# Kernel optimization log

Hardware: AMD Instinct MI355X
Metric: run time of the kernel (lower is better)

The kernel has to match this reference:

```python
import jax, jax.numpy as jnp
import numpy as np

B, T, V, E, M, L = 1024, 64, 1024, 512, 1024, 32
PE, PO = M // 2, (M - 1) // 2  # even/odd pair counts


def complex_normalize(x, eps=1e-8):
    mag = jnp.sqrt((x.real ** 2 + x.imag ** 2).sum(-1, keepdims=True) + eps)
    return x / mag


def pair_unitary(v0, v1, t, p, r):
    # 2x2 MZI unitary applied to pairs (v0, v1); t/p/r are (P,) broadcast over batch
    c, s = jnp.cos(t), jnp.sin(t)
    eip, eir = jnp.exp(1j * p), jnp.exp(1j * r)
    u11 = eip * c * eir
    u12 = eip * (1j * s)
    u21 = (1j * s) * eir
    u22 = c
    return u11 * v0 + u12 * v1, u21 * v0 + u22 * v1


def setup_inputs() -> dict:
    key = jax.random.key(0)
    ks = jax.random.split(key, 16)
    sE = 1.0 / np.sqrt(E)
    return {
        "context_tokens": jax.random.randint(ks[0], (B, T), 0, V),
        "embed": 0.02 * jax.random.normal(ks[1], (V, E), jnp.float32),
        "W_ih": sE * jax.random.normal(ks[2], (3 * E, E), jnp.float32),
        "W_hh": sE * jax.random.normal(ks[3], (3 * E, E), jnp.float32),
        "b_ih": jnp.zeros((3 * E,), jnp.float32),
        "b_hh": jnp.zeros((3 * E,), jnp.float32),
        "Wc": 0.02 * jax.random.normal(ks[4], (2 * M, E), jnp.float32),
        "bc": jnp.zeros((2 * M,), jnp.float32),
        "phase": 0.1 * jax.random.normal(ks[5], (L, M), jnp.float32),
        "theta_e": 0.1 * jax.random.normal(ks[6], (L, PE), jnp.float32),
        "phi_e": 0.1 * jax.random.normal(ks[7], (L, PE), jnp.float32),
        "rho_e": 0.1 * jax.random.normal(ks[8], (L, PE), jnp.float32),
        "theta_o": 0.1 * jax.random.normal(ks[9], (L, PO), jnp.float32),
        "phi_o": 0.1 * jax.random.normal(ks[10], (L, PO), jnp.float32),
        "rho_o": 0.1 * jax.random.normal(ks[11], (L, PO), jnp.float32),
        "R_real": 0.01 * jax.random.normal(ks[12], (V, M), jnp.float32),
        "R_imag": 0.01 * jax.random.normal(ks[13], (V, M), jnp.float32),
    }


def reference(context_tokens, embed, W_ih, W_hh, b_ih, b_hh, Wc, bc,
              phase, theta_e, phi_e, rho_e, theta_o, phi_o, rho_o,
              R_real, R_imag):
    # --- ContextEncoder: embedding + GRU (torch gate order r,z,n) ---
    x = embed[context_tokens]                      # (B,T,E)
    x_gates = x @ W_ih.T + b_ih                    # (B,T,3E) precomputed input gates

    def gru_step(h, xg):
        ir, iz, in_ = jnp.split(xg, 3, axis=-1)
        hr, hz, hn = jnp.split(h @ W_hh.T + b_hh, 3, axis=-1)
        r = jax.nn.sigmoid(ir + hr)
        z = jax.nn.sigmoid(iz + hz)
        n = jnp.tanh(in_ + r * hn)
        return (1.0 - z) * n + z * h, None

    h0 = jnp.zeros((x.shape[0], embed.shape[1]), x.dtype)
    h, _ = jax.lax.scan(gru_step, h0, jnp.swapaxes(x_gates, 0, 1))  # (B,E)

    zc = h @ Wc.T + bc                              # (B,2M)
    re, im = jnp.split(zc, 2, axis=-1)
    psi = complex_normalize(re + 1j * im)           # (B,M) complex64

    # --- QuantumCore: stack of MZI layers ---
    def layer(psi, p):
        ph, te, pe, re_, to, po, ro = p
        psi = psi * jnp.exp(1j * ph)
        D = psi.shape[1]
        # even pairs (0,1),(2,3),...
        v0, v1 = pair_unitary(psi[:, 0::2], psi[:, 1::2], te, pe, re_)
        psi = psi.at[:, 0::2].set(v0).at[:, 1::2].set(v1)
        # odd pairs (1,2),(3,4),...
        v0, v1 = pair_unitary(psi[:, 1:D - 1:2], psi[:, 2:D:2], to, po, ro)
        psi = psi.at[:, 1:D - 1:2].set(v0).at[:, 2:D:2].set(v1)
        return complex_normalize(psi), None

    psi, _ = jax.lax.scan(layer, psi, (phase, theta_e, phi_e, rho_e,
                                       theta_o, phi_o, rho_o))

    # --- QuantumReadout: Born rule log-probs ---
    R = R_real + 1j * R_imag                        # (V,M)
    amps = psi @ R.T                                # (B,V) complex
    log_mag_sq = jnp.log(amps.real ** 2 + amps.imag ** 2 + 1e-12)
    return log_mag_sq - jax.scipy.special.logsumexp(log_mag_sq, axis=-1, keepdims=True)
```

## Files before the change

### kernel.cpp

```cpp
#include <hip/hip_runtime.h>
#include <math.h>

typedef __bf16 bf16_t;
typedef bf16_t bf16x8 __attribute__((ext_vector_type(8)));
typedef float  f32x4  __attribute__((ext_vector_type(4)));

#define B_  1024
#define T_  64
#define V_  1024
#define E_  512
#define M_  1024
#define L_  32
#define PE_ 512
#define PO_ 511
#define G3_ 1536
#define M2_ 2048

#define MFMA_BF16 __builtin_amdgcn_mfma_f32_16x16x32_bf16

__device__ __forceinline__ void stage16f(float* lds_base, const float* gsrc) {
  __builtin_amdgcn_global_load_lds(
      (const __attribute__((address_space(1))) unsigned int*)gsrc,
      (__attribute__((address_space(3))) unsigned int*)lds_base, 16, 0, 0);
}

__device__ __forceinline__ size_t tiled_off(int row, int k) {
  return ((size_t)(row >> 4) * 16 + (k >> 5)) * 512 +
         (size_t)(((k >> 3) & 3) * 16 + (row & 15)) * 8 + (k & 7);
}

__device__ __forceinline__ void split_chunk(const float* __restrict__ src,
                                            bf16_t* __restrict__ hi,
                                            bf16_t* __restrict__ lo, int blk,
                                            int tid) {
  int i4 = (blk * 256 + tid) * 4;
  float4 v = *(const float4*)&src[i4];
  float vv[4] = {v.x, v.y, v.z, v.w};
#pragma unroll
  for (int j = 0; j < 4; j++) {
    bf16_t h = (bf16_t)vv[j];
    hi[i4 + j] = h;
    lo[i4 + j] = (bf16_t)(vv[j] - (float)h);
  }
}

__global__ __launch_bounds__(256) void prep_all(
    const float* __restrict__ embed, bf16_t* __restrict__ emb_hi,
    bf16_t* __restrict__ emb_lo, const float* __restrict__ W_ih,
    bf16_t* __restrict__ wih_hi, bf16_t* __restrict__ wih_lo,
    const float* __restrict__ Wc, bf16_t* __restrict__ wc_hi,
    bf16_t* __restrict__ wc_lo, const float* __restrict__ R_real,
    bf16_t* __restrict__ rr_hi, bf16_t* __restrict__ rr_lo,
    const float* __restrict__ R_imag, bf16_t* __restrict__ ri_hi,
    bf16_t* __restrict__ ri_lo, const float* __restrict__ W_hh,
    bf16_t* __restrict__ Wp_hi, bf16_t* __restrict__ Wp_lo,
    const float* __restrict__ phase, const float* __restrict__ th_e,
    const float* __restrict__ ph_e, const float* __restrict__ rh_e,
    float* __restrict__ Uep, const float* __restrict__ th_o,
    const float* __restrict__ ph_o, const float* __restrict__ rh_o,
    float* __restrict__ Uop) {
  const int bid = blockIdx.x, tid = threadIdx.x;
  if (bid < 512) {
    split_chunk(embed, emb_hi, emb_lo, bid, tid);
  } else if (bid < 1280) {
    split_chunk(W_ih, wih_hi, wih_lo, bid - 512, tid);
  } else if (bid < 2304) {
    split_chunk(Wc, wc_hi, wc_lo, bid - 1280, tid);
  } else if (bid < 3328) {
    split_chunk(R_real, rr_hi, rr_lo, bid - 2304, tid);
  } else if (bid < 4352) {
    split_chunk(R_imag, ri_hi, ri_lo, bid - 3328, tid);
  } else if (bid < 5888) {
    int q = bid - 4352;
    int c = q / 96, loc = q % 96;
    int g = loc >> 5, el = loc & 31;
    const float* src = &W_hh[(size_t)(g * 512 + c * 32 + el) * 512];
    if (tid < 64) {
      int k0 = tid * 8;
      float4 v0 = *(const float4*)&src[k0];
      float4 v1 = *(const float4*)&src[k0 + 4];
      float vv[8] = {v0.x, v0.y, v0.z, v0.w, v1.x, v1.y, v1.z, v1.w};
      bf16x8 h8, l8;
#pragma unroll
      for (int j = 0; j < 8; j++) {
        bf16_t h = (bf16_t)vv[j];
        h8[j] = h;
        l8[j] = (bf16_t)(vv[j] - (float)h);
      }
      size_t toff = tiled_off(q, k0);
      *(bf16x8*)&Wp_hi[toff] = h8;
      *(bf16x8*)&Wp_lo[toff] = l8;
    }
  } else if (bid < 5952) {
    int idx = (bid - 5888) * 256 + tid;
    if (idx < L_ * PE_) {
      int l = idx >> 9, p = idx & 511;
      float t = th_e[idx], pp = ph_e[idx], r = rh_e[idx];
      float c = cosf(t), s = sinf(t);
      float cp = cosf(pp), sp = sinf(pp), cr = cosf(r), sr = sinf(r);
      float u11r = c * (cp * cr - sp * sr), u11i = c * (cp * sr + sp * cr);
      float u12r = -s * sp, u12i = s * cp;
      float u21r = -s * sr, u21i = s * cr;
      float u22r = c, u22i = 0.0f;
      float f0 = phase[l * M_ + 2 * p], f1 = phase[l * M_ + 2 * p + 1];
      float c0 = cosf(f0), s0 = sinf(f0), c1 = cosf(f1), s1 = sinf(f1);
      float a, b;
      a = u11r * c0 - u11i * s0; b = u11r * s0 + u11i * c0; u11r = a; u11i = b;
      a = u21r * c0 - u21i * s0; b = u21r * s0 + u21i * c0; u21r = a; u21i = b;
      a = u12r * c1 - u12i * s1; b = u12r * s1 + u12i * c1; u12r = a; u12i = b;
      a = u22r * c1 - u22i * s1; b = u22r * s1 + u22i * c1; u22r = a; u22i = b;
      int j = p & 3, ln = (p >> 2) & 63, hh = p >> 8;
      size_t base = (size_t)l * 4096 + (size_t)(j * 4 + hh) * 256 + ln * 4;
      *(float4*)&Uep[base]       = make_float4(u11r, u11i, u12r, u12i);
      *(float4*)&Uep[base + 512] = make_float4(u21r, u21i, u22r, u22i);
    }
  } else {
    int idx = (bid - 5952) * 256 + tid;
    if (idx < L_ * PO_) {
      int l = idx / PO_, p = idx % PO_;
      float t = th_o[idx], pp = ph_o[idx], r = rh_o[idx];
      float c = cosf(t), s = sinf(t);
      float cp = cosf(pp), sp = sinf(pp), cr = cosf(r), sr = sinf(r);
      int j = p & 3, ln = (p >> 2) & 63, hh = p >> 8;
      size_t base = (size_t)l * 4096 + (size_t)(j * 4 + hh) * 256 + ln * 4;
      *(float4*)&Uop[base] = make_float4(c * (cp * cr - sp * sr),
                                         c * (cp * sr + sp * cr), -s * sp,
                                         s * cp);
      *(float4*)&Uop[base + 512] = make_float4(-s * sr, s * cr, c, 0.0f);
    }
  }
}

__global__ __launch_bounds__(256) void gemm_bt_mfma_split(
    const bf16_t* __restrict__ Ah, const bf16_t* __restrict__ Al,
    const bf16_t* __restrict__ Bh, const bf16_t* __restrict__ Bl,
    float* __restrict__ C, int Ndim, int K) {
  __shared__ bf16_t sAh[64 * 32], sAl[64 * 32], sBh[64 * 32], sBl[64 * 32];
  const int tid = threadIdx.x;
  const int m0 = blockIdx.y * 64, n0 = blockIdx.x * 64;
  const int wave = tid >> 6, lane = tid & 63;
  const int wr = wave >> 1, wc = wave & 1;
  const int quad = lane >> 4, l16 = lane & 15;
  f32x4 acc[2][2] = {};
  const int srow = tid >> 2, sk = (tid & 3) * 8;

  for (int k0 = 0; k0 < K; k0 += 32) {
    bf16x8 ah = *(const bf16x8*)&Ah[(size_t)(m0 + srow) * K + k0 + sk];
    bf16x8 al = *(const bf16x8*)&Al[(size_t)(m0 + srow) * K + k0 + sk];
    bf16x8 bh = *(const bf16x8*)&Bh[(size_t)(n0 + srow) * K + k0 + sk];
    bf16x8 bl = *(const bf16x8*)&Bl[(size_t)(n0 + srow) * K + k0 + sk];
    __syncthreads();
    *(bf16x8*)&sAh[srow * 32 + sk] = ah;
    *(bf16x8*)&sAl[srow * 32 + sk] = al;
    *(bf16x8*)&sBh[srow * 32 + sk] = bh;
    *(bf16x8*)&sBl[srow * 32 + sk] = bl;
    __syncthreads();
    bf16x8 fAh[2], fAl[2], fBh[2], fBl[2];
#pragma unroll
    for (int i = 0; i < 2; i++) {
      fAh[i] = *(const bf16x8*)&sAh[(wr * 32 + i * 16 + l16) * 32 + quad * 8];
      fAl[i] = *(const bf16x8*)&sAl[(wr * 32 + i * 16 + l16) * 32 + quad * 8];
      fBh[i] = *(const bf16x8*)&sBh[(wc * 32 + i * 16 + l16) * 32 + quad * 8];
      fBl[i] = *(const bf16x8*)&sBl[(wc * 32 + i * 16 + l16) * 32 + quad * 8];
    }
#pragma unroll
    for (int i = 0; i < 2; i++)
#pragma unroll
      for (int j = 0; j < 2; j++) {
        acc[i][j] = MFMA_BF16(fAh[i], fBh[j], acc[i][j], 0, 0, 0);
        acc[i][j] = MFMA_BF16(fAh[i], fBl[j], acc[i][j], 0, 0, 0);
        acc[i][j] = MFMA_BF16(fAl[i], fBh[j], acc[i][j], 0, 0, 0);
      }
  }
#pragma unroll
  for (int i = 0; i < 2; i++)
#pragma unroll
    for (int j = 0; j < 2; j++)
#pragma unroll
      for (int r = 0; r < 4; r++) {
        int row = wr * 32 + i * 16 + quad * 4 + r;
        int col = wc * 32 + j * 16 + l16;
        C[(size_t)(m0 + row) * Ndim + n0 + col] = acc[i][j][r];
      }
}

__global__ __launch_bounds__(512) void gru_step10(
    const bf16_t* __restrict__ Hh, const bf16_t* __restrict__ Hl,
    const bf16_t* __restrict__ Wph, const bf16_t* __restrict__ Wpl,
    const int* __restrict__ tok, const float* __restrict__ eg,
    const float* __restrict__ b_ih, const float* __restrict__ b_hh,
    bf16_t* __restrict__ Oh, bf16_t* __restrict__ Ol, int t, int final_) {
  __shared__ float sC[2][64 * 100];
  __shared__ float sbih[96], sbhh[96];
  const int tid = threadIdx.x;
  const int g = tid >> 8;
  const int gtid = tid & 255;
  const int ct = blockIdx.y, m0 = blockIdx.x * 64;
  const int n0e = ct * 32;
  const int wg = gtid >> 6, lane = tid & 63;
  const int wr = wg >> 1, wc = wg & 1;
  const int quad = lane >> 4, l16 = lane & 15;

  if (tid < 96) {
    sbih[tid] = b_ih[(tid >> 5) * 512 + n0e + (tid & 31)];
    sbhh[tid] = b_hh[(tid >> 5) * 512 + n0e + (tid & 31)];
  }

  float pir[4], piz[4], pin[4], phv[4];
#pragma unroll
  for (int u = 0; u < 4; u++) {
    int flat = u * 512 + tid;
    int row = flat >> 5, el = flat & 31;
    int bb = m0 + row, eG = n0e + el;
    int tk = tok[bb * T_ + t];
    pir[u] = eg[(size_t)tk * G3_ + eG];
    piz[u] = eg[(size_t)tk * G3_ + 512 + eG];
    pin[u] = eg[(size_t)tk * G3_ + 1024 + eG];
    size_t toff = tiled_off(bb, eG);
    phv[u] = (float)Hh[toff] + (float)Hl[toff];
  }

  const size_t aB0 = (size_t)((m0 >> 4) + wr * 2 + 0) * 8192 + (size_t)g * 4096 + lane * 8;
  const size_t aB1 = (size_t)((m0 >> 4) + wr * 2 + 1) * 8192 + (size_t)g * 4096 + lane * 8;
  const size_t bB0 = (size_t)(ct * 6 + wc * 3 + 0) * 8192 + (size_t)g * 4096 + lane * 8;
  const size_t bB1 = (size_t)(ct * 6 + wc * 3 + 1) * 8192 + (size_t)g * 4096 + lane * 8;
  const size_t bB2 = (size_t)(ct * 6 + wc * 3 + 2) * 8192 + (size_t)g * 4096 + lane * 8;

  f32x4 acc[2][3] = {};
#pragma unroll
  for (int kb = 0; kb < 8; ++kb) {
    const int ko = kb * 512;
    bf16x8 fah[2], fal[2], fbh[3], fbl[3];
    fah[0] = *(const bf16x8*)&Hh[aB0 + ko];
    fah[1] = *(const bf16x8*)&Hh[aB1 + ko];
    fal[0] = *(const bf16x8*)&Hl[aB0 + ko];
    fal[1] = *(const bf16x8*)&Hl[aB1 + ko];
    fbh[0] = *(const bf16x8*)&Wph[bB0 + ko];
    fbh[1] = *(const bf16x8*)&Wph[bB1 + ko];
    fbh[2] = *(const bf16x8*)&Wph[bB2 + ko];
    fbl[0] = *(const bf16x8*)&Wpl[bB0 + ko];
    fbl[1] = *(const bf16x8*)&Wpl[bB1 + ko];
    fbl[2] = *(const bf16x8*)&Wpl[bB2 + ko];
#pragma unroll
    for (int i = 0; i < 2; i++)
#pragma unroll
      for (int j = 0; j < 3; j++) {
        acc[i][j] = MFMA_BF16(fah[i], fbh[j], acc[i][j], 0, 0, 0);
        acc[i][j] = MFMA_BF16(fah[i], fbl[j], acc[i][j], 0, 0, 0);
        acc[i][j] = MFMA_BF16(fal[i], fbh[j], acc[i][j], 0, 0, 0);
      }
  }
#pragma unroll
  for (int i = 0; i < 2; i++)
#pragma unroll
    for (int j = 0; j < 3; j++)
#pragma unroll
      for (int r = 0; r < 4; r++)
        sC[g][(wr * 32 + i * 16 + quad * 4 + r) * 100 + wc * 48 + j * 16 + l16] =
            acc[i][j][r];
  __syncthreads();
#pragma unroll
  for (int u = 0; u < 4; u++) {
    int flat = u * 512 + tid;
    int row = flat >> 5, el = flat & 31;
    int bb = m0 + row, eG = n0e + el;
    float ir = pir[u] + sbih[el];
    float iz = piz[u] + sbih[32 + el];
    float in_ = pin[u] + sbih[64 + el];
    float hr = sC[0][row * 100 + el] + sC[1][row * 100 + el] + sbhh[el];
    float hz = sC[0][row * 100 + 32 + el] + sC[1][row * 100 + 32 + el] + sbhh[32 + el];
    float hn = sC[0][row * 100 + 64 + el] + sC[1][row * 100 + 64 + el] + sbhh[64 + el];
    float r = 1.0f / (1.0f + __expf(-(ir + hr)));
    float z = 1.0f / (1.0f + __expf(-(iz + hz)));
    float targ = fminf(fmaxf(in_ + r * hn, -15.0f), 15.0f);
    float e2 = __expf(2.0f * targ);
    float n = (e2 - 1.0f) / (e2 + 1.0f);
    float hnew = (1.0f - z) * n + z * phv[u];
    bf16_t hh = (bf16_t)hnew;
    bf16_t ll = (bf16_t)(hnew - (float)hh);
    if (final_) {
      size_t hidx = (size_t)bb * 512 + eG;
      Oh[hidx] = hh;
      Ol[hidx] = ll;
    } else {
      size_t toff = tiled_off(bb, eG);
      Oh[toff] = hh;
      Ol[toff] = ll;
    }
  }
}

__device__ inline void apply_u(float4 A, float4 Bv, float& x0r, float& x0i,
                               float& x1r, float& x1i) {
  float n0r = A.x * x0r - A.y * x0i + A.z * x1r - A.w * x1i;
  float n0i = A.x * x0i + A.y * x0r + A.z * x1i + A.w * x1r;
  float n1r = Bv.x * x0r - Bv.y * x0i + Bv.z * x1r - Bv.w * x1i;
  float n1i = Bv.x * x0i + Bv.y * x0r + Bv.z * x1i + Bv.w * x1r;
  x0r = n0r; x0i = n0i; x1r = n1r; x1i = n1i;
}

__global__ __launch_bounds__(512) void qc5(
    const float* __restrict__ zc, const float* __restrict__ bc,
    const float* __restrict__ Uep, const float* __restrict__ Uop,
    bf16_t* __restrict__ prh, bf16_t* __restrict__ prl,
    bf16_t* __restrict__ pih, bf16_t* __restrict__ pil) {
  __shared__ float sU[2][8192];
  __shared__ float sred[8];
  __shared__ float4 sEx[2][4][2];
  const int tid = threadIdx.x;
  const int wave = tid >> 6, lane = tid & 63;
  const int wb = wave >> 1, h = wave & 1;
  const int b = blockIdx.x * 4 + wb;
  const int e0 = h * 512 + lane * 8;

#define STAGE_L(l, buf)                                                       \
  {                                                                           \
    _Pragma("unroll") for (int r = 0; r < 4; r++) {                           \
      int c = wave * 4 + r;                                                   \
      const float* src = (c < 16)                                             \
          ? &Uep[(size_t)(l) * 4096 + c * 256 + lane * 4]                     \
          : &Uop[(size_t)(l) * 4096 + (c - 16) * 256 + lane * 4];             \
      stage16f(&sU[buf][c * 256], src);                                       \
    }                                                                         \
  }

  float xr[8], xi[8];
  {
    const float4* zr4 = (const float4*)&zc[(size_t)b * M2_ + e0];
    const float4* zi4 = (const float4*)&zc[(size_t)b * M2_ + M_ + e0];
    const float4* br4 = (const float4*)&bc[e0];
    const float4* bi4 = (const float4*)&bc[M_ + e0];
#pragma unroll
    for (int q = 0; q < 2; q++) {
      float4 a = zr4[q], bb = br4[q];
      xr[4 * q + 0] = a.x + bb.x; xr[4 * q + 1] = a.y + bb.y;
      xr[4 * q + 2] = a.z + bb.z; xr[4 * q + 3] = a.w + bb.w;
      float4 c2 = zi4[q], d = bi4[q];
      xi[4 * q + 0] = c2.x + d.x; xi[4 * q + 1] = c2.y + d.y;
      xi[4 * q + 2] = c2.z + d.z; xi[4 * q + 3] = c2.w + d.w;
    }
  }
  STAGE_L(0, 0);
  {
    float s = 0.0f;
#pragma unroll
    for (int k = 0; k < 8; k++) s += xr[k] * xr[k] + xi[k] * xi[k];
    for (int off = 32; off; off >>= 1) s += __shfl_xor(s, off);
    if (lane == 0) sred[wave] = s;
    __syncthreads();
    float inv = 1.0f / sqrtf(sred[2 * wb] + sred[2 * wb + 1] + 1e-8f);
#pragma unroll
    for (int k = 0; k < 8; k++) { xr[k] *= inv; xi[k] *= inv; }
  }
  if (h == 0 && lane == 63) sEx[0][wb][0] = make_float4(xr[6], xi[6], xr[7], xi[7]);
  if (h == 1 && lane == 0)  sEx[0][wb][1] = make_float4(xr[0], xi[0], xr[1], xi[1]);
  __syncthreads();

#pragma unroll 1
  for (int l = 0; l < L_; ++l) {
    const int buf = l & 1;
    if (l + 1 < L_) STAGE_L(l + 1, 1 - buf);
    const float* Ub = &sU[buf][0];
    const float* Ob = &sU[buf][4096];
    float4 par = make_float4(0.f, 0.f, 0.f, 0.f);
    if (h == 0 && lane == 63) par = sEx[buf][wb][1];
    if (h == 1 && lane == 0)  par = sEx[buf][wb][0];
#pragma unroll
    for (int j = 0; j < 4; j++) {
      float4 A  = *(const float4*)&Ub[(j * 4 + h) * 256 + lane * 4];
      float4 Bv = *(const float4*)&Ub[(j * 4 + 2 + h) * 256 + lane * 4];
      apply_u(A, Bv, xr[2 * j], xi[2 * j], xr[2 * j + 1], xi[2 * j + 1]);
    }
    float exr = 0.f, exi = 0.f;
    if (h == 0 && lane == 63) {
      float4 Ae = *(const float4*)&Ub[1 * 256];
      exr = Ae.x * par.x - Ae.y * par.y + Ae.z * par.z - Ae.w * par.w;
      exi = Ae.x * par.y + Ae.y * par.x + Ae.z * par.w + Ae.w * par.z;
    }
    if (h == 1 && lane == 0) {
      float4 Be = *(const float4*)&Ub[14 * 256 + 252];
      exr = Be.x * par.x - Be.y * par.y + Be.z * par.z - Be.w * par.w;
      exi = Be.x * par.y + Be.y * par.x + Be.z * par.w + Be.w * par.z;
    }
#pragma unroll
    for (int j = 0; j < 3; j++) {
      float4 A  = *(const float4*)&Ob[(j * 4 + h) * 256 + lane * 4];
      float4 Bv = *(const float4*)&Ob[(j * 4 + 2 + h) * 256 + lane * 4];
      apply_u(A, Bv, xr[2 * j + 1], xi[2 * j + 1], xr[2 * j + 2], xi[2 * j + 2]);
    }
    float nr = __shfl_down(xr[0], 1), ni = __shfl_down(xi[0], 1);
    if (h == 0 && lane == 63) { nr = exr; ni = exi; }
    float srr = 0.f, sii = 0.f;
    if (!(h == 1 && lane == 63)) {
      float4 A3 = *(const float4*)&Ob[(12 + h) * 256 + lane * 4];
      float4 B3 = *(const float4*)&Ob[(14 + h) * 256 + lane * 4];
      float n0r = A3.x * xr[7] - A3.y * xi[7] + A3.z * nr - A3.w * ni;
      float n0i = A3.x * xi[7] + A3.y * xr[7] + A3.z * ni + A3.w * nr;
      srr = B3.x * xr[7] - B3.y * xi[7] + B3.z * nr - B3.w * ni;
      sii = B3.x * xi[7] + B3.y * xr[7] + B3.z * ni + B3.w * nr;
      xr[7] = n0r; xi[7] = n0i;
    }
    float nx0r = 0.f, nx0i = 0.f;
    if (h == 1 && lane == 0) {
      float4 Bc = *(const float4*)&Ob[14 * 256 + 252];
      nx0r = Bc.x * exr - Bc.y * exi + Bc.z * xr[0] - Bc.w * xi[0];
      nx0i = Bc.x * exi + Bc.y * exr + Bc.z * xi[0] + Bc.w * xr[0];
    }
    float rr = __shfl_up(srr, 1), ri2 = __shfl_up(sii, 1);
    if (lane > 0) { xr[0] = rr; xi[0] = ri2; }
    if (h == 1 && lane == 0) { xr[0] = nx0r; xi[0] = nx0i; }
    if (h == 0 && lane == 63)
      sEx[1 - buf][wb][0] = make_float4(xr[6], xi[6], xr[7], xi[7]);
    if (h == 1 && lane == 0)
      sEx[1 - buf][wb][1] = make_float4(xr[0], xi[0], xr[1], xi[1]);
    __syncthreads();
  }
#undef STAGE_L
  size_t base = (size_t)b * M_ + e0;
  bf16x8 vh, vl, wh, wl;
#pragma unroll
  for (int k = 0; k < 8; k++) {
    float vr = xr[k], vi = xi[k];
    bf16_t h1 = (bf16_t)vr;
    vh[k] = h1; vl[k] = (bf16_t)(vr - (float)h1);
    bf16_t h2 = (bf16_t)vi;
    wh[k] = h2; wl[k] = (bf16_t)(vi - (float)h2);
  }
  *(bf16x8*)&prh[base] = vh;
  *(bf16x8*)&prl[base] = vl;
  *(bf16x8*)&pih[base] = wh;
  *(bf16x8*)&pil[base] = wl;
}

__global__ __launch_bounds__(256) void readout_mfma(
    const bf16_t* __restrict__ Arh, const bf16_t* __restrict__ Arl,
    const bf16_t* __restrict__ Aih, const bf16_t* __restrict__ Ail,
    const bf16_t* __restrict__ Brh, const bf16_t* __restrict__ Brl,
    const bf16_t* __restrict__ Bih, const bf16_t* __restrict__ Bil,
    float* __restrict__ out) {
  __shared__ bf16_t sArh[64 * 32], sArl[64 * 32], sAih[64 * 32], sAil[64 * 32];
  __shared__ bf16_t sBrh[64 * 32], sBrl[64 * 32], sBih[64 * 32], sBil[64 * 32];
  const int tid = threadIdx.x;
  const int b0 = blockIdx.y * 64, v0 = blockIdx.x * 64;
  const int wave = tid >> 6, lane = tid & 63;
  const int wr = wave >> 1, wc = wave & 1;
  const int quad = lane >> 4, l16 = lane & 15;
  f32x4 aP[2][2] = {}, aQ[2][2] = {}, aI[2][2] = {};
  const int srow = tid >> 2, sk = (tid & 3) * 8;

  for (int k0 = 0; k0 < M_; k0 += 32) {
    size_t aoff = (size_t)(b0 + srow) * M_ + k0 + sk;
    size_t boff = (size_t)(v0 + srow) * M_ + k0 + sk;
    bf16x8 v0r = *(const bf16x8*)&Arh[aoff];
    bf16x8 v1r = *(const bf16x8*)&Arl[aoff];
    bf16x8 v2r = *(const bf16x8*)&Aih[aoff];
    bf16x8 v3r = *(const bf16x8*)&Ail[aoff];
    bf16x8 v4r = *(const bf16x8*)&Brh[boff];
    bf16x8 v5r = *(const bf16x8*)&Brl[boff];
    bf16x8 v6r = *(const bf16x8*)&Bih[boff];
    bf16x8 v7r = *(const bf16x8*)&Bil[boff];
    __syncthreads();
    *(bf16x8*)&sArh[srow * 32 + sk] = v0r;
    *(bf16x8*)&sArl[srow * 32 + sk] = v1r;
    *(bf16x8*)&sAih[srow * 32 + sk] = v2r;
    *(bf16x8*)&sAil[srow * 32 + sk] = v3r;
    *(bf16x8*)&sBrh[srow * 32 + sk] = v4r;
    *(bf16x8*)&sBrl[srow * 32 + sk] = v5r;
    *(bf16x8*)&sBih[srow * 32 + sk] = v6r;
    *(bf16x8*)&sBil[srow * 32 + sk] = v7r;
    __syncthreads();
    bf16x8 fArh[2], fArl[2], fAih[2], fAil[2], fBrh[2], fBrl[2], fBih[2], fBil[2];
#pragma unroll
    for (int i = 0; i < 2; i++) {
      int ra = (wr * 32 + i * 16 + l16) * 32 + quad * 8;
      int rb = (wc * 32 + i * 16 + l16) * 32 + quad * 8;
      fArh[i] = *(const bf16x8*)&sArh[ra];
      fArl[i] = *(const bf16x8*)&sArl[ra];
      fAih[i] = *(const bf16x8*)&sAih[ra];
      fAil[i] = *(const bf16x8*)&sAil[ra];
      fBrh[i] = *(const bf16x8*)&sBrh[rb];
      fBrl[i] = *(const bf16x8*)&sBrl[rb];
      fBih[i] = *(const bf16x8*)&sBih[rb];
      fBil[i] = *(const bf16x8*)&sBil[rb];
    }
#pragma unroll
    for (int i = 0; i < 2; i++)
#pragma unroll
      for (int j = 0; j < 2; j++) {
        aP[i][j] = MFMA_BF16(fArh[i], fBrh[j], aP[i][j], 0, 0, 0);
        aP[i][j] = MFMA_BF16(fArh[i], fBrl[j], aP[i][j], 0, 0, 0);
        aP[i][j] = MFMA_BF16(fArl[i], fBrh[j], aP[i][j], 0, 0, 0);
        aQ[i][j] = MFMA_BF16(fAih[i], fBih[j], aQ[i][j], 0, 0, 0);
        aQ[i][j] = MFMA_BF16(fAih[i], fBil[j], aQ[i][j], 0, 0, 0);
        aQ[i][j] = MFMA_BF16(fAil[i], fBih[j], aQ[i][j], 0, 0, 0);
        aI[i][j] = MFMA_BF16(fArh[i], fBih[j], aI[i][j], 0, 0, 0);
        aI[i][j] = MFMA_BF16(fArh[i], fBil[j], aI[i][j], 0, 0, 0);
        aI[i][j] = MFMA_BF16(fArl[i], fBih[j], aI[i][j], 0, 0, 0);
        aI[i][j] = MFMA_BF16(fAih[i], fBrh[j], aI[i][j], 0, 0, 0);
        aI[i][j] = MFMA_BF16(fAih[i], fBrl[j], aI[i][j], 0, 0, 0);
        aI[i][j] = MFMA_BF16(fAil[i], fBrh[j], aI[i][j], 0, 0, 0);
      }
  }
#pragma unroll
  for (int i = 0; i < 2; i++)
#pragma unroll
    for (int j = 0; j < 2; j++)
#pragma unroll
      for (int r = 0; r < 4; r++) {
        int row = wr * 32 + i * 16 + quad * 4 + r;
        int col = wc * 32 + j * 16 + l16;
        float re = aP[i][j][r] - aQ[i][j][r];
        float im = aI[i][j][r];
        out[(size_t)(b0 + row) * V_ + v0 + col] = logf(re * re + im * im + 1e-12f);
      }
}

__global__ __launch_bounds__(256) void lse_kernel(float* __restrict__ out) {
  __shared__ float redm[4], reds[4];
  const int b = blockIdx.x, t = threadIdx.x;
  float4 v = *(float4*)&out[(size_t)b * V_ + 4 * t];
  float mx = fmaxf(fmaxf(v.x, v.y), fmaxf(v.z, v.w));
  for (int off = 32; off; off >>= 1) mx = fmaxf(mx, __shfl_down(mx, off, 64));
  if ((t & 63) == 0) redm[t >> 6] = mx;
  __syncthreads();
  mx = fmaxf(fmaxf(redm[0], redm[1]), fmaxf(redm[2], redm[3]));
  float s = expf(v.x - mx) + expf(v.y - mx) + expf(v.z - mx) + expf(v.w - mx);
  for (int off = 32; off; off >>= 1) s += __shfl_down(s, off, 64);
  if ((t & 63) == 0) reds[t >> 6] = s;
  __syncthreads();
  s = reds[0] + reds[1] + reds[2] + reds[3];
  float lse = mx + logf(s);
  v.x -= lse; v.y -= lse; v.z -= lse; v.w -= lse;
  *(float4*)&out[(size_t)b * V_ + 4 * t] = v;
}

extern "C" void kernel_launch(void* const* d_in, const int* in_sizes, int n_in,
                              void* d_out, int out_size, void* d_ws, size_t ws_size,
                              hipStream_t stream) {
  const int*   tokens = (const int*)d_in[0];
  const float* embed  = (const float*)d_in[1];
  const float* W_ih   = (const float*)d_in[2];
  const float* W_hh   = (const float*)d_in[3];
  const float* b_ih   = (const float*)d_in[4];
  const float* b_hh   = (const float*)d_in[5];
  const float* Wc     = (const float*)d_in[6];
  const float* bc     = (const float*)d_in[7];
  const float* phase  = (const float*)d_in[8];
  const float* theta_e = (const float*)d_in[9];
  const float* phi_e  = (const float*)d_in[10];
  const float* rho_e  = (const float*)d_in[11];
  const float* theta_o = (const float*)d_in[12];
  const float* phi_o  = (const float*)d_in[13];
  const float* rho_o  = (const float*)d_in[14];
  const float* R_real = (const float*)d_in[15];
  const float* R_imag = (const float*)d_in[16];
  float* out = (float*)d_out;

  char* w = (char*)d_ws;
  auto alloc = [&](size_t bytes) -> void* {
    void* p = (void*)w;
    w += (bytes + 255) & ~(size_t)255;
    return p;
  };
  char* region0 = w;
  bf16_t* emb_hi = (bf16_t*)alloc((size_t)V_ * E_ * 2);
  bf16_t* emb_lo = (bf16_t*)alloc((size_t)V_ * E_ * 2);
  bf16_t* wih_hi = (bf16_t*)alloc((size_t)G3_ * E_ * 2);
  bf16_t* wih_lo = (bf16_t*)alloc((size_t)G3_ * E_ * 2);
  bf16_t* wc_hi  = (bf16_t*)alloc((size_t)M2_ * E_ * 2);
  bf16_t* wc_lo  = (bf16_t*)alloc((size_t)M2_ * E_ * 2);
  char* region1 = w;
  float*  eg     = (float*)alloc((size_t)V_ * G3_ * 4);
  bf16_t* Wp_hi  = (bf16_t*)alloc((size_t)G3_ * E_ * 2);
  bf16_t* Wp_lo  = (bf16_t*)alloc((size_t)G3_ * E_ * 2);
  bf16_t* h0_hi = (bf16_t*)alloc((size_t)B_ * E_ * 2);
  bf16_t* h0_lo = (bf16_t*)alloc((size_t)B_ * E_ * 2);
  bf16_t* h1_hi = (bf16_t*)alloc((size_t)B_ * E_ * 2);
  bf16_t* h1_lo = (bf16_t*)alloc((size_t)B_ * E_ * 2);
  bf16_t* rr_hi = (bf16_t*)alloc((size_t)V_ * M_ * 2);
  bf16_t* rr_lo = (bf16_t*)alloc((size_t)V_ * M_ * 2);
  bf16_t* ri_hi = (bf16_t*)alloc((size_t)V_ * M_ * 2);
  bf16_t* ri_lo = (bf16_t*)alloc((size_t)V_ * M_ * 2);
  float*  Uep   = (float*)alloc((size_t)L_ * 4096 * 4);
  float*  Uop   = (float*)alloc((size_t)L_ * 4096 * 4);

  float*  zc  = (float*)region1;
  bf16_t* prh = (bf16_t*)(region0 + 0 * 2097152);
  bf16_t* prl = (bf16_t*)(region0 + 1 * 2097152);
  bf16_t* pih = (bf16_t*)(region0 + 2 * 2097152);
  bf16_t* pil = (bf16_t*)(region0 + 3 * 2097152);

  hipMemsetAsync(h0_hi, 0, (size_t)B_ * E_ * 2 * 2, stream);

  prep_all<<<6016, 256, 0, stream>>>(
      embed, emb_hi, emb_lo, W_ih, wih_hi, wih_lo, Wc, wc_hi, wc_lo, R_real,
      rr_hi, rr_lo, R_imag, ri_hi, ri_lo, W_hh, Wp_hi, Wp_lo, phase, theta_e,
      phi_e, rho_e, Uep, theta_o, phi_o, rho_o, Uop);

  {
    dim3 grid(G3_ / 64, V_ / 64);
    gemm_bt_mfma_split<<<grid, 256, 0, stream>>>(emb_hi, emb_lo, wih_hi, wih_lo,
                                                 eg, G3_, E_);
  }

  for (int t = 0; t < T_; ++t) {
    const bf16_t* ih = (t & 1) ? h1_hi : h0_hi;
    const bf16_t* il = (t & 1) ? h1_lo : h0_lo;
    bf16_t* oh = (t & 1) ? h0_hi : h1_hi;
    bf16_t* ol = (t & 1) ? h0_lo : h1_lo;
    dim3 grid(16, 16);
    gru_step10<<<grid, 512, 0, stream>>>(ih, il, Wp_hi, Wp_lo, tokens, eg,
                                         b_ih, b_hh, oh, ol, t,
                                         (t == T_ - 1) ? 1 : 0);
  }

  {
    dim3 grid(M2_ / 64, B_ / 64);
    gemm_bt_mfma_split<<<grid, 256, 0, stream>>>(h0_hi, h0_lo, wc_hi, wc_lo,
                                                 zc, M2_, E_);
  }

  qc5<<<B_ / 4, 512, 0, stream>>>(zc, bc, Uep, Uop, prh, prl, pih, pil);

  {
    dim3 grid(V_ / 64, B_ / 64);
    readout_mfma<<<grid, 256, 0, stream>>>(prh, prl, pih, pil, rr_hi, rr_lo,
                                           ri_hi, ri_lo, out);
  }

  lse_kernel<<<B_, 256, 0, stream>>>(out);
}
```

Measured before the change: 907.9 us.

## Stage GRU recurrent weights through double-buffered LDS and halve QC block size

The GRU step kernel now copies its W_hh hi/lo weight fragments into a double-buffered shared-memory tile with async global-to-LDS loads. The next k-chunk is prefetched while the current one is multiplied, where before each wave read the weights straight from global memory. This adds extra barriers and about 96KB more LDS per block, which may lower occupancy. The quantum-core kernel also moves to 256-thread blocks covering 2 batch rows instead of 4, doubling the block count so more blocks are in flight.

After: 862.5 us. 1.05x faster.

```diff
diff --git a/kernel.cpp b/kernel.cpp
--- a/kernel.cpp
+++ b/kernel.cpp
@@ -19,6 +19,11 @@
 #define MFMA_BF16 __builtin_amdgcn_mfma_f32_16x16x32_bf16
 
 __device__ __forceinline__ void stage16f(float* lds_base, const float* gsrc) {
+  __builtin_amdgcn_global_load_lds(
+      (const __attribute__((address_space(1))) unsigned int*)gsrc,
+      (__attribute__((address_space(3))) unsigned int*)lds_base, 16, 0, 0);
+}
+__device__ __forceinline__ void stage16b(bf16_t* lds_base, const bf16_t* gsrc) {
   __builtin_amdgcn_global_load_lds(
       (const __attribute__((address_space(1))) unsigned int*)gsrc,
       (__attribute__((address_space(3))) unsigned int*)lds_base, 16, 0, 0);
@@ -184,12 +189,13 @@
       }
 }
 
-__global__ __launch_bounds__(512) void gru_step10(
+__global__ __launch_bounds__(512) void gru_step11(
     const bf16_t* __restrict__ Hh, const bf16_t* __restrict__ Hl,
     const bf16_t* __restrict__ Wph, const bf16_t* __restrict__ Wpl,
     const int* __restrict__ tok, const float* __restrict__ eg,
     const float* __restrict__ b_ih, const float* __restrict__ b_hh,
     bf16_t* __restrict__ Oh, bf16_t* __restrict__ Ol, int t, int final_) {
+  __shared__ bf16_t sB[2][2][24 * 512];
   __shared__ float sC[2][64 * 100];
   __shared__ float sbih[96], sbhh[96];
   const int tid = threadIdx.x;
@@ -201,6 +207,21 @@
   const int wr = wg >> 1, wc = wg & 1;
   const int quad = lane >> 4, l16 = lane & 15;
 
+#define STAGE_B(buf, it)                                                      \
+  {                                                                           \
+    _Pragma("unroll") for (int r = 0; r < 6; r++) {                           \
+      int c = wg * 6 + r;                                                     \
+      int f = (c >= 12) ? (c - 12) : c;                                       \
+      int j = f >> 1, ks = f & 1;                                             \
+      const bf16_t* srcp = (c < 12) ? Wph : Wpl;                              \
+      stage16b(&sB[buf][g][c * 512],                                          \
+               &srcp[(size_t)(ct * 6 + j) * 8192 +                            \
+                     (size_t)(g * 8 + (it) * 2 + ks) * 512 + lane * 8]);      \
+    }                                                                         \
+  }
+
+  STAGE_B(0, 0);
+
   if (tid < 96) {
     sbih[tid] = b_ih[(tid >> 5) * 512 + n0e + (tid & 31)];
     sbhh[tid] = b_hh[(tid >> 5) * 512 + n0e + (tid & 31)];
@@ -222,34 +243,41 @@
 
   const size_t aB0 = (size_t)((m0 >> 4) + wr * 2 + 0) * 8192 + (size_t)g * 4096 + lane * 8;
   const size_t aB1 = (size_t)((m0 >> 4) + wr * 2 + 1) * 8192 + (size_t)g * 4096 + lane * 8;
-  const size_t bB0 = (size_t)(ct * 6 + wc * 3 + 0) * 8192 + (size_t)g * 4096 + lane * 8;
-  const size_t bB1 = (size_t)(ct * 6 + wc * 3 + 1) * 8192 + (size_t)g * 4096 + lane * 8;
-  const size_t bB2 = (size_t)(ct * 6 + wc * 3 + 2) * 8192 + (size_t)g * 4096 + lane * 8;
 
   f32x4 acc[2][3] = {};
-#pragma unroll
-  for (int kb = 0; kb < 8; ++kb) {
-    const int ko = kb * 512;
-    bf16x8 fah[2], fal[2], fbh[3], fbl[3];
-    fah[0] = *(const bf16x8*)&Hh[aB0 + ko];
-    fah[1] = *(const bf16x8*)&Hh[aB1 + ko];
-    fal[0] = *(const bf16x8*)&Hl[aB0 + ko];
-    fal[1] = *(const bf16x8*)&Hl[aB1 + ko];
-    fbh[0] = *(const bf16x8*)&Wph[bB0 + ko];
-    fbh[1] = *(const bf16x8*)&Wph[bB1 + ko];
-    fbh[2] = *(const bf16x8*)&Wph[bB2 + ko];
-    fbl[0] = *(const bf16x8*)&Wpl[bB0 + ko];
-    fbl[1] = *(const bf16x8*)&Wpl[bB1 + ko];
-    fbl[2] = *(const bf16x8*)&Wpl[bB2 + ko];
-#pragma unroll
-    for (int i = 0; i < 2; i++)
+  __syncthreads();
+#pragma unroll
+  for (int it = 0; it < 4; ++it) {
+    const int buf = it & 1;
+    if (it < 3) STAGE_B(buf ^ 1, it + 1);
+    const bf16_t* sBg = &sB[buf][g][0];
+#pragma unroll
+    for (int ks2 = 0; ks2 < 2; ++ks2) {
+      const int kb = it * 2 + ks2;
+      const int ko = kb * 512;
+      bf16x8 fah[2], fal[2], fbh[3], fbl[3];
+      fah[0] = *(const bf16x8*)&Hh[aB0 + ko];
+      fah[1] = *(const bf16x8*)&Hh[aB1 + ko];
+      fal[0] = *(const bf16x8*)&Hl[aB0 + ko];
+      fal[1] = *(const bf16x8*)&Hl[aB1 + ko];
 #pragma unroll
       for (int j = 0; j < 3; j++) {
-        acc[i][j] = MFMA_BF16(fah[i], fbh[j], acc[i][j], 0, 0, 0);
-        acc[i][j] = MFMA_BF16(fah[i], fbl[j], acc[i][j], 0, 0, 0);
-        acc[i][j] = MFMA_BF16(fal[i], fbh[j], acc[i][j], 0, 0, 0);
+        int f = (wc * 3 + j) * 2 + ks2;
+        fbh[j] = *(const bf16x8*)&sBg[f * 512 + lane * 8];
+        fbl[j] = *(const bf16x8*)&sBg[(f + 12) * 512 + lane * 8];
       }
-  }
+#pragma unroll
+      for (int i = 0; i < 2; i++)
+#pragma unroll
+        for (int j = 0; j < 3; j++) {
+          acc[i][j] = MFMA_BF16(fah[i], fbh[j], acc[i][j], 0, 0, 0);
+          acc[i][j] = MFMA_BF16(fah[i], fbl[j], acc[i][j], 0, 0, 0);
+          acc[i][j] = MFMA_BF16(fal[i], fbh[j], acc[i][j], 0, 0, 0);
+        }
+    }
+    __syncthreads();
+  }
+#undef STAGE_B
 #pragma unroll
   for (int i = 0; i < 2; i++)
 #pragma unroll
@@ -299,24 +327,24 @@
   x0r = n0r; x0i = n0i; x1r = n1r; x1i = n1i;
 }
 
-__global__ __launch_bounds__(512) void qc5(
+__global__ __launch_bounds__(256) void qc6(
     const float* __restrict__ zc, const float* __restrict__ bc,
     const float* __restrict__ Uep, const float* __restrict__ Uop,
     bf16_t* __restrict__ prh, bf16_t* __restrict__ prl,
     bf16_t* __restrict__ pih, bf16_t* __restrict__ pil) {
   __shared__ float sU[2][8192];
-  __shared__ float sred[8];
-  __shared__ float4 sEx[2][4][2];
+  __shared__ float sred[4];
+  __shared__ float4 sEx[2][2][2];
   const int tid = threadIdx.x;
   const int wave = tid >> 6, lane = tid & 63;
   const int wb = wave >> 1, h = wave & 1;
-  const int b = blockIdx.x * 4 + wb;
+  const int b = blockIdx.x * 2 + wb;
   const int e0 = h * 512 + lane * 8;
 
 #define STAGE_L(l, buf)                                                       \
   {                                                                           \
-    _Pragma("unroll") for (int r = 0; r < 4; r++) {                           \
-      int c = wave * 4 + r;                                                   \
+    _Pragma("unroll") for (int r = 0; r < 8; r++) {                           \
+      int c = wave * 8 + r;                                                   \
       const float* src = (c < 16)                                             \
           ? &Uep[(size_t)(l) * 4096 + c * 256 + lane * 4]                     \
           : &Uop[(size_t)(l) * 4096 + (c - 16) * 256 + lane * 4];             \
@@ -609,7 +637,7 @@
     bf16_t* oh = (t & 1) ? h0_hi : h1_hi;
     bf16_t* ol = (t & 1) ? h0_lo : h1_lo;
     dim3 grid(16, 16);
-    gru_step10<<<grid, 512, 0, stream>>>(ih, il, Wp_hi, Wp_lo, tokens, eg,
+    gru_step11<<<grid, 512, 0, stream>>>(ih, il, Wp_hi, Wp_lo, tokens, eg,
                                          b_ih, b_hh, oh, ol, t,
                                          (t == T_ - 1) ? 1 : 0);
   }
@@ -620,7 +648,7 @@
                                                  zc, M2_, E_);
   }
 
-  qc5<<<B_ / 4, 512, 0, stream>>>(zc, bc, Uep, Uop, prh, prl, pih, pil);
+  qc6<<<B_ / 2, 256, 0, stream>>>(zc, bc, Uep, Uop, prh, prl, pih, pil);
 
   {
     dim3 grid(V_ / 64, B_ / 64);
```
